# Performance work log

Measured on AMD Instinct MI355X. Metric: run time of the kernel, lower is better.

Reference implementation:

```python
import jax, jax.numpy as jnp
import numpy as np

RBF_CO = 10.077141124806595


def setup_inputs() -> dict:
    key = jax.random.key(0)
    k1, k2, k3 = jax.random.split(key, 3)
    n, dim = 2048, 128
    N, out_dim = 50000, 64
    features = jax.random.normal(k1, (n, dim), dtype=jnp.float32)
    train_data = jax.random.normal(k2, (N, dim), dtype=jnp.float32)
    weights = jax.random.normal(k3, (N, out_dim), dtype=jnp.float32) * 0.02
    return {"features": features, "train_data": train_data, "weights": weights}


def reference(features, train_data, weights):
    x2 = jnp.sum(features * features, axis=-1, keepdims=True)      # [n, 1]
    t2 = jnp.sum(train_data * train_data, axis=-1)                 # [N]
    d2 = x2 + t2[None, :] - 2.0 * (features @ train_data.T)        # [n, N]
    dist = jnp.sqrt(jnp.maximum(d2, 0.0))                          # clamp fp error
    k = jnp.exp(-dist / RBF_CO / 2.0)                              # RBF kernel [n, N]
    return k @ weights                                              # [n, out_dim]
```

## Files before the change

### kernel.cpp

```cpp
#include <hip/hip_runtime.h>
#include <hip/hip_bf16.h>
#include <stdint.h>

#define DIM 128
#define ODIM 64
#define BM 128
#define BN 64
#define NSPLIT 48
#define SPROW 72

typedef __attribute__((ext_vector_type(8))) __bf16 bf16x8;
typedef __attribute__((ext_vector_type(2))) __bf16 bf16x2;
typedef __attribute__((ext_vector_type(4))) float f32x4;

#define MFMA16(a, b, c) __builtin_amdgcn_mfma_f32_16x16x32_bf16((a), (b), (c), 0, 0, 0)

#define RBFD 10.077141124806595
#define LOG2E 1.4426950408889634
#define C2D ((LOG2E / (2.0 * RBFD)) * (LOG2E / (2.0 * RBFD)))

__device__ __forceinline__ void async_copy16(const void* g, void* l) {
  __builtin_amdgcn_global_load_lds((const __attribute__((address_space(1))) void*)g,
                                   (__attribute__((address_space(3))) void*)l, 16, 0, 0);
}
__device__ __forceinline__ void async_copy4(const void* g, void* l) {
  __builtin_amdgcn_global_load_lds((const __attribute__((address_space(1))) void*)g,
                                   (__attribute__((address_space(3))) void*)l, 4, 0, 0);
}

__device__ __forceinline__ uint32_t pack_bf16(float a, float b) {
  uint32_t ua = __builtin_bit_cast(uint32_t, a) + 0x8000u;
  uint32_t ub = __builtin_bit_cast(uint32_t, b) + 0x8000u;
  return __builtin_amdgcn_perm(ub, ua, 0x07060302u);
}

__global__ void prep_rows(const float* __restrict__ train, __bf16* __restrict__ Tb,
                          float* __restrict__ t2, const float* __restrict__ feat,
                          __bf16* __restrict__ Fb, float* __restrict__ x2,
                          int Ntrain, int NpadTrain, int nFeat, int trainBlocks, float scale) {
  int b = blockIdx.x;
  const float* src;
  __bf16* dst;
  float* sq;
  int nValid, nPad, row0;
  float padv;
  if (b < trainBlocks) {
    src = train; dst = Tb; sq = t2; nValid = Ntrain; nPad = NpadTrain; row0 = b * 4; padv = 1e30f;
  } else {
    src = feat; dst = Fb; sq = x2; nValid = nFeat; nPad = nFeat; row0 = (b - trainBlocks) * 4; padv = 0.0f;
  }
  int row = row0 + (threadIdx.x >> 6);
  int lane = threadIdx.x & 63;
  if (row >= nPad) return;
  float2 v = make_float2(0.0f, 0.0f);
  if (row < nValid) v = ((const float2*)src)[(size_t)row * 64 + lane];
  bf16x2 p;
  p.x = (__bf16)v.x;
  p.y = (__bf16)v.y;
  *(bf16x2*)&dst[(size_t)row * DIM + lane * 2] = p;
  float ss = v.x * v.x + v.y * v.y;
  #pragma unroll
  for (int off = 32; off > 0; off >>= 1) ss += __shfl_down(ss, off);
  if (lane == 0) sq[row] = (row < nValid) ? ss * scale : padv;
}

__global__ void transpose_weights(const float* __restrict__ W, __bf16* __restrict__ Wt,
                                  int N, int Npad) {
  __shared__ float tile[64][65];
  int j0 = (int)blockIdx.x * 64;
  int t = threadIdx.x;
  int jr = t >> 2;
  int cg = (t & 3) * 16;
  int j = j0 + jr;
  if (j < N) {
    const float4* src = (const float4*)(W + (size_t)j * ODIM);
    #pragma unroll
    for (int q = 0; q < 4; ++q) {
      float4 u = src[(cg >> 2) + q];
      tile[jr][cg + q * 4 + 0] = u.x;
      tile[jr][cg + q * 4 + 1] = u.y;
      tile[jr][cg + q * 4 + 2] = u.z;
      tile[jr][cg + q * 4 + 3] = u.w;
    }
  } else {
    #pragma unroll
    for (int q = 0; q < 16; ++q) tile[jr][cg + q] = 0.0f;
  }
  __syncthreads();
  int v = t >> 2;
  int jc = (t & 3) * 16;
  __bf16 ob[16];
  #pragma unroll
  for (int q = 0; q < 16; ++q) ob[q] = (__bf16)tile[jc + q][v];
  __bf16* dst = Wt + (size_t)v * Npad + j0 + jc;
  *(bf16x8*)dst = *(bf16x8*)&ob[0];
  *(bf16x8*)(dst + 8) = *(bf16x8*)&ob[8];
}

template <bool ATOMIC>
__global__ __launch_bounds__(256, 3) void rbf_main(
    const __bf16* __restrict__ Fb, const __bf16* __restrict__ Tb,
    const __bf16* __restrict__ Wt, const float* __restrict__ t2g,
    const float* __restrict__ x2g, float* __restrict__ outOrPart,
    int nRows, int Npad, int nChunks) {
  __shared__ __bf16 sT[BN * DIM];
  __shared__ __bf16 sW[ODIM * BN];
  __shared__ __bf16 sP[BM * SPROW];
  __shared__ float st2[BN];

  const int tid = threadIdx.x;
  const int wave = tid >> 6;
  const int lane = tid & 63;
  const int l16 = lane & 15;
  const int g4 = lane >> 4;

  const int ns = (int)blockIdx.x;
  const int mb = (int)blockIdx.y;

  constexpr float KNEG2 = (float)(-2.0 * C2D);

  bf16x8 bF[2][4];
  #pragma unroll
  for (int nf = 0; nf < 2; ++nf)
    #pragma unroll
    for (int ko = 0; ko < 4; ++ko)
      bF[nf][ko] = *(const bf16x8*)(Fb + ((size_t)(mb * BM + wave * 32 + nf * 16 + l16)) * DIM +
                                    ko * 32 + g4 * 8);

  float x2v[2];
  #pragma unroll
  for (int nf = 0; nf < 2; ++nf)
    x2v[nf] = x2g[mb * BM + wave * 32 + nf * 16 + l16];

  f32x4 zero4 = {0.0f, 0.0f, 0.0f, 0.0f};
  f32x4 oacc[2][4];
  #pragma unroll
  for (int mo = 0; mo < 2; ++mo)
    #pragma unroll
    for (int vi = 0; vi < 4; ++vi) oacc[mo][vi] = zero4;

  for (int c = ns; c < nChunks; c += NSPLIT) {
    const int n0 = c * BN;

    {
      const char* gT = (const char*)Tb + (size_t)n0 * 256;
      #pragma unroll
      for (int i = 0; i < 4; ++i) {
        int off = i * 4096 + wave * 1024;
        int loff = off + lane * 16;
        int row = loff >> 8;
        int gran = (loff >> 4) & 15;
        async_copy16(gT + row * 256 + ((gran ^ (row & 15)) << 4), (char*)sT + off);
      }
    }
    {
      #pragma unroll
      for (int i = 0; i < 2; ++i) {
        int off = i * 4096 + wave * 1024;
        int loff = off + lane * 16;
        int v = loff >> 7;
        int gran = (loff >> 4) & 7;
        const char* gW = (const char*)Wt + ((size_t)v * Npad + n0) * 2 + ((gran ^ (v & 7)) << 4);
        async_copy16(gW, (char*)sW + off);
      }
    }
    if (wave == 0) async_copy4((const char*)(t2g + n0) + lane * 4, (char*)st2);
    __syncthreads();

    f32x4 sacc[4][2];
    #pragma unroll
    for (int mt = 0; mt < 4; ++mt)
      #pragma unroll
      for (int nf = 0; nf < 2; ++nf) sacc[mt][nf] = zero4;

    #pragma unroll
    for (int ko = 0; ko < 4; ++ko) {
      bf16x8 a[4];
      #pragma unroll
      for (int mt = 0; mt < 4; ++mt) {
        int row = mt * 16 + l16;
        int slot = (ko * 4 + g4) ^ l16;
        a[mt] = *(const bf16x8*)((const char*)sT + row * 256 + (slot << 4));
      }
      #pragma unroll
      for (int mt = 0; mt < 4; ++mt)
        #pragma unroll
        for (int nf = 0; nf < 2; ++nf)
          sacc[mt][nf] = MFMA16(a[mt], bF[nf][ko], sacc[mt][nf]);
    }

    #pragma unroll
    for (int mt = 0; mt < 4; ++mt) {
      f32x4 t2v = *(const f32x4*)&st2[mt * 16 + g4 * 4];
      #pragma unroll
      for (int nf = 0; nf < 2; ++nf) {
        f32x4 s = sacc[mt][nf];
        float kv[4];
        #pragma unroll
        for (int r = 0; r < 4; ++r) {
          float d2 = __builtin_fmaf(KNEG2, s[r], t2v[r] + x2v[nf]);
          d2 = fmaxf(d2, 0.0f);
          kv[r] = __builtin_amdgcn_exp2f(-__builtin_amdgcn_sqrtf(d2));
        }
        uint32_t lo = pack_bf16(kv[0], kv[1]);
        uint32_t hi = pack_bf16(kv[2], kv[3]);
        uint2* dst = (uint2*)&sP[(wave * 32 + nf * 16 + l16) * SPROW + mt * 16 + g4 * 4];
        *dst = make_uint2(lo, hi);
      }
    }

    #pragma unroll
    for (int ko2 = 0; ko2 < 2; ++ko2) {
      bf16x8 p[2];
      #pragma unroll
      for (int mo = 0; mo < 2; ++mo)
        p[mo] = *(const bf16x8*)&sP[(wave * 32 + mo * 16 + l16) * SPROW + ko2 * 32 + g4 * 8];
      bf16x8 w[4];
      #pragma unroll
      for (int vi = 0; vi < 4; ++vi) {
        int v = vi * 16 + l16;
        int slot = (ko2 * 4 + g4) ^ (l16 & 7);
        w[vi] = *(const bf16x8*)((const char*)sW + v * 128 + (slot << 4));
      }
      #pragma unroll
      for (int mo = 0; mo < 2; ++mo)
        #pragma unroll
        for (int vi = 0; vi < 4; ++vi)
          oacc[mo][vi] = MFMA16(p[mo], w[vi], oacc[mo][vi]);
    }
    __syncthreads();
  }

  if (ATOMIC) {
    float* out = outOrPart;
    #pragma unroll
    for (int mo = 0; mo < 2; ++mo)
      #pragma unroll
      for (int vi = 0; vi < 4; ++vi)
        #pragma unroll
        for (int r = 0; r < 4; ++r) {
          int row = mb * BM + wave * 32 + mo * 16 + g4 * 4 + r;
          int col = vi * 16 + l16;
          atomicAdd(&out[(size_t)row * ODIM + col], oacc[mo][vi][r]);
        }
  } else {
    float* dst = outOrPart + (size_t)ns * (size_t)nRows * ODIM;
    #pragma unroll
    for (int mo = 0; mo < 2; ++mo)
      #pragma unroll
      for (int vi = 0; vi < 4; ++vi)
        #pragma unroll
        for (int r = 0; r < 4; ++r) {
          int row = mb * BM + wave * 32 + mo * 16 + g4 * 4 + r;
          int col = vi * 16 + l16;
          dst[(size_t)row * ODIM + col] = oacc[mo][vi][r];
        }
  }
}

__global__ void reduce_parts(const float4* __restrict__ part, float4* __restrict__ out,
                             int total4) {
  int i = (int)blockIdx.x * blockDim.x + threadIdx.x;
  if (i >= total4) return;
  float4 s = make_float4(0.0f, 0.0f, 0.0f, 0.0f);
  #pragma unroll
  for (int sp = 0; sp < NSPLIT; ++sp) {
    float4 v = part[(size_t)sp * total4 + i];
    s.x += v.x; s.y += v.y; s.z += v.z; s.w += v.w;
  }
  out[i] = s;
}

extern "C" void kernel_launch(void* const* d_in, const int* in_sizes, int n_in,
                              void* d_out, int out_size, void* d_ws, size_t ws_size,
                              hipStream_t stream) {
  (void)n_in;
  const float* features = (const float*)d_in[0];
  const float* train = (const float*)d_in[1];
  const float* weights = (const float*)d_in[2];
  float* out = (float*)d_out;

  const int n = in_sizes[0] / DIM;
  const int N = in_sizes[1] / DIM;
  const int Npad = ((N + 63) / 64) * 64;
  const int nChunks = Npad / 64;

  size_t off = 0;
  auto alloc = [&](size_t bytes) {
    size_t o = off;
    off = (off + bytes + 255) & ~(size_t)255;
    return o;
  };
  size_t oT = alloc((size_t)Npad * DIM * 2);
  size_t oW = alloc((size_t)ODIM * Npad * 2);
  size_t oF = alloc((size_t)n * DIM * 2);
  size_t ot2 = alloc((size_t)Npad * 4);
  size_t ox2 = alloc((size_t)n * 4);
  size_t oPart = alloc((size_t)NSPLIT * n * ODIM * 4);
  size_t needFull = off;

  char* ws = (char*)d_ws;
  __bf16* Tb = (__bf16*)(ws + oT);
  __bf16* Wt = (__bf16*)(ws + oW);
  __bf16* Fb = (__bf16*)(ws + oF);
  float* t2 = (float*)(ws + ot2);
  float* x2 = (float*)(ws + ox2);

  const float scale = (float)C2D;
  const int trainBlocks = Npad / 4;
  prep_rows<<<trainBlocks + n / 4, 256, 0, stream>>>(train, Tb, t2, features, Fb, x2,
                                                     N, Npad, n, trainBlocks, scale);
  transpose_weights<<<Npad / 64, 256, 0, stream>>>(weights, Wt, N, Npad);

  const int mBlocks = n / BM;
  dim3 grid(NSPLIT, mBlocks);

  if (ws_size >= needFull) {
    float* part = (float*)(ws + oPart);
    rbf_main<false><<<grid, 256, 0, stream>>>(Fb, Tb, Wt, t2, x2, part, n, Npad, nChunks);
    int total4 = n * ODIM / 4;
    reduce_parts<<<(total4 + 255) / 256, 256, 0, stream>>>((const float4*)part, (float4*)out,
                                                           total4);
  } else {
    hipMemsetAsync(d_out, 0, (size_t)out_size * sizeof(float), stream);
    rbf_main<true><<<grid, 256, 0, stream>>>(Fb, Tb, Wt, t2, x2, out, n, Npad, nChunks);
  }
}
```

Baseline: 146.0 us.

## Feed RBF kernel values from registers into second MFMA, drop LDS staging

Removes the shared-memory round trip for the bf16 kernel matrix by packing exp results in registers and feeding them directly as A operands of 16x16x16 MFMAs, relying on the accumulator layout matching the operand layout. This frees LDS, allowing occupancy to be raised to 4 blocks per CU, and the split count is raised to 64 with grid axes swapped. The preprocessing and weight transpose kernels are merged into one launch. The clamp of d2 to zero is dropped, risking NaN from sqrt of small negative values.

```diff
diff --git a/kernel.cpp b/kernel.cpp
--- a/kernel.cpp
+++ b/kernel.cpp
@@ -6,14 +6,15 @@
 #define ODIM 64
 #define BM 128
 #define BN 64
-#define NSPLIT 48
-#define SPROW 72
+#define NSPLIT 64
 
 typedef __attribute__((ext_vector_type(8))) __bf16 bf16x8;
+typedef __attribute__((ext_vector_type(4))) __bf16 bf16x4;
 typedef __attribute__((ext_vector_type(2))) __bf16 bf16x2;
 typedef __attribute__((ext_vector_type(4))) float f32x4;
 
-#define MFMA16(a, b, c) __builtin_amdgcn_mfma_f32_16x16x32_bf16((a), (b), (c), 0, 0, 0)
+#define MFMA_K32(a, b, c) __builtin_amdgcn_mfma_f32_16x16x32_bf16((a), (b), (c), 0, 0, 0)
+#define MFMA_K16(a, b, c) __builtin_amdgcn_mfma_f32_16x16x16bf16_1k((a), (b), (c), 0, 0, 0)
 
 #define RBFD 10.077141124806595
 #define LOG2E 1.4426950408889634
@@ -34,45 +35,45 @@
   return __builtin_amdgcn_perm(ub, ua, 0x07060302u);
 }
 
-__global__ void prep_rows(const float* __restrict__ train, __bf16* __restrict__ Tb,
-                          float* __restrict__ t2, const float* __restrict__ feat,
-                          __bf16* __restrict__ Fb, float* __restrict__ x2,
-                          int Ntrain, int NpadTrain, int nFeat, int trainBlocks, float scale) {
+__global__ void prep_all(const float* __restrict__ train, __bf16* __restrict__ Tb,
+                         float* __restrict__ t2, const float* __restrict__ feat,
+                         __bf16* __restrict__ Fb, float* __restrict__ x2,
+                         const float* __restrict__ W, __bf16* __restrict__ Wt,
+                         int Ntrain, int Npad, int nFeat, int tB, int fB, float scale) {
+  __shared__ float tile[64][65];
   int b = blockIdx.x;
-  const float* src;
-  __bf16* dst;
-  float* sq;
-  int nValid, nPad, row0;
-  float padv;
-  if (b < trainBlocks) {
-    src = train; dst = Tb; sq = t2; nValid = Ntrain; nPad = NpadTrain; row0 = b * 4; padv = 1e30f;
-  } else {
-    src = feat; dst = Fb; sq = x2; nValid = nFeat; nPad = nFeat; row0 = (b - trainBlocks) * 4; padv = 0.0f;
-  }
-  int row = row0 + (threadIdx.x >> 6);
-  int lane = threadIdx.x & 63;
-  if (row >= nPad) return;
-  float2 v = make_float2(0.0f, 0.0f);
-  if (row < nValid) v = ((const float2*)src)[(size_t)row * 64 + lane];
-  bf16x2 p;
-  p.x = (__bf16)v.x;
-  p.y = (__bf16)v.y;
-  *(bf16x2*)&dst[(size_t)row * DIM + lane * 2] = p;
-  float ss = v.x * v.x + v.y * v.y;
-  #pragma unroll
-  for (int off = 32; off > 0; off >>= 1) ss += __shfl_down(ss, off);
-  if (lane == 0) sq[row] = (row < nValid) ? ss * scale : padv;
-}
-
-__global__ void transpose_weights(const float* __restrict__ W, __bf16* __restrict__ Wt,
-                                  int N, int Npad) {
-  __shared__ float tile[64][65];
-  int j0 = (int)blockIdx.x * 64;
   int t = threadIdx.x;
+  if (b < tB + fB) {
+    const float* src;
+    __bf16* dst;
+    float* sq;
+    int nValid, nPad, row0;
+    float padv;
+    if (b < tB) {
+      src = train; dst = Tb; sq = t2; nValid = Ntrain; nPad = Npad; row0 = b * 4; padv = 1e30f;
+    } else {
+      src = feat; dst = Fb; sq = x2; nValid = nFeat; nPad = nFeat; row0 = (b - tB) * 4; padv = 0.0f;
+    }
+    int row = row0 + (t >> 6);
+    int lane = t & 63;
+    if (row >= nPad) return;
+    float2 v = make_float2(0.0f, 0.0f);
+    if (row < nValid) v = ((const float2*)src)[(size_t)row * 64 + lane];
+    bf16x2 p;
+    p.x = (__bf16)v.x;
+    p.y = (__bf16)v.y;
+    *(bf16x2*)&dst[(size_t)row * DIM + lane * 2] = p;
+    float ss = v.x * v.x + v.y * v.y;
+    #pragma unroll
+    for (int off = 32; off > 0; off >>= 1) ss += __shfl_down(ss, off);
+    if (lane == 0) sq[row] = (row < nValid) ? ss * scale : padv;
+    return;
+  }
+  int j0 = (b - tB - fB) * 64;
   int jr = t >> 2;
   int cg = (t & 3) * 16;
   int j = j0 + jr;
-  if (j < N) {
+  if (j < Ntrain) {
     const float4* src = (const float4*)(W + (size_t)j * ODIM);
     #pragma unroll
     for (int q = 0; q < 4; ++q) {
@@ -98,14 +99,13 @@
 }
 
 template <bool ATOMIC>
-__global__ __launch_bounds__(256, 3) void rbf_main(
+__global__ __launch_bounds__(256, 4) void rbf_main(
     const __bf16* __restrict__ Fb, const __bf16* __restrict__ Tb,
     const __bf16* __restrict__ Wt, const float* __restrict__ t2g,
     const float* __restrict__ x2g, float* __restrict__ outOrPart,
     int nRows, int Npad, int nChunks) {
   __shared__ __bf16 sT[BN * DIM];
   __shared__ __bf16 sW[ODIM * BN];
-  __shared__ __bf16 sP[BM * SPROW];
   __shared__ float st2[BN];
 
   const int tid = threadIdx.x;
@@ -114,8 +114,8 @@
   const int l16 = lane & 15;
   const int g4 = lane >> 4;
 
-  const int ns = (int)blockIdx.x;
-  const int mb = (int)blockIdx.y;
+  const int mb = (int)blockIdx.x;
+  const int ns = (int)blockIdx.y;
 
   constexpr float KNEG2 = (float)(-2.0 * C2D);
 
@@ -135,9 +135,9 @@
   f32x4 zero4 = {0.0f, 0.0f, 0.0f, 0.0f};
   f32x4 oacc[2][4];
   #pragma unroll
-  for (int mo = 0; mo < 2; ++mo)
-    #pragma unroll
-    for (int vi = 0; vi < 4; ++vi) oacc[mo][vi] = zero4;
+  for (int nf = 0; nf < 2; ++nf)
+    #pragma unroll
+    for (int vi = 0; vi < 4; ++vi) oacc[nf][vi] = zero4;
 
   for (int c = ns; c < nChunks; c += NSPLIT) {
     const int n0 = c * BN;
@@ -167,66 +167,40 @@
     if (wave == 0) async_copy4((const char*)(t2g + n0) + lane * 4, (char*)st2);
     __syncthreads();
 
-    f32x4 sacc[4][2];
-    #pragma unroll
-    for (int mt = 0; mt < 4; ++mt)
-      #pragma unroll
-      for (int nf = 0; nf < 2; ++nf) sacc[mt][nf] = zero4;
-
-    #pragma unroll
-    for (int ko = 0; ko < 4; ++ko) {
-      bf16x8 a[4];
+    uint2 pk[4][2];
+    #pragma unroll
+    for (int mt = 0; mt < 4; ++mt) {
+      f32x4 s0 = zero4, s1 = zero4;
+      #pragma unroll
+      for (int ko = 0; ko < 4; ++ko) {
+        int slot = (ko * 4 + g4) ^ l16;
+        bf16x8 a = *(const bf16x8*)((const char*)sT + (mt * 16 + l16) * 256 + (slot << 4));
+        s0 = MFMA_K32(a, bF[0][ko], s0);
+        s1 = MFMA_K32(a, bF[1][ko], s1);
+      }
+      f32x4 t2v = *(const f32x4*)&st2[mt * 16 + g4 * 4];
+      float kv0[4], kv1[4];
+      #pragma unroll
+      for (int r = 0; r < 4; ++r) {
+        float d20 = __builtin_fmaf(KNEG2, s0[r], t2v[r] + x2v[0]);
+        float d21 = __builtin_fmaf(KNEG2, s1[r], t2v[r] + x2v[1]);
+        kv0[r] = __builtin_amdgcn_exp2f(-__builtin_amdgcn_sqrtf(d20));
+        kv1[r] = __builtin_amdgcn_exp2f(-__builtin_amdgcn_sqrtf(d21));
+      }
+      pk[mt][0] = make_uint2(pack_bf16(kv0[0], kv0[1]), pack_bf16(kv0[2], kv0[3]));
+      pk[mt][1] = make_uint2(pack_bf16(kv1[0], kv1[1]), pack_bf16(kv1[2], kv1[3]));
+    }
+
+    #pragma unroll
+    for (int vi = 0; vi < 4; ++vi) {
+      int rowB = (vi * 16 + l16) * 128 + ((g4 & 1) << 3);
       #pragma unroll
       for (int mt = 0; mt < 4; ++mt) {
-        int row = mt * 16 + l16;
-        int slot = (ko * 4 + g4) ^ l16;
-        a[mt] = *(const bf16x8*)((const char*)sT + row * 256 + (slot << 4));
-      }
-      #pragma unroll
-      for (int mt = 0; mt < 4; ++mt)
-        #pragma unroll
-        for (int nf = 0; nf < 2; ++nf)
-          sacc[mt][nf] = MFMA16(a[mt], bF[nf][ko], sacc[mt][nf]);
-    }
-
-    #pragma unroll
-    for (int mt = 0; mt < 4; ++mt) {
-      f32x4 t2v = *(const f32x4*)&st2[mt * 16 + g4 * 4];
-      #pragma unroll
-      for (int nf = 0; nf < 2; ++nf) {
-        f32x4 s = sacc[mt][nf];
-        float kv[4];
-        #pragma unroll
-        for (int r = 0; r < 4; ++r) {
-          float d2 = __builtin_fmaf(KNEG2, s[r], t2v[r] + x2v[nf]);
-          d2 = fmaxf(d2, 0.0f);
-          kv[r] = __builtin_amdgcn_exp2f(-__builtin_amdgcn_sqrtf(d2));
-        }
-        uint32_t lo = pack_bf16(kv[0], kv[1]);
-        uint32_t hi = pack_bf16(kv[2], kv[3]);
-        uint2* dst = (uint2*)&sP[(wave * 32 + nf * 16 + l16) * SPROW + mt * 16 + g4 * 4];
-        *dst = make_uint2(lo, hi);
-      }
-    }
-
-    #pragma unroll
-    for (int ko2 = 0; ko2 < 2; ++ko2) {
-      bf16x8 p[2];
-      #pragma unroll
-      for (int mo = 0; mo < 2; ++mo)
-        p[mo] = *(const bf16x8*)&sP[(wave * 32 + mo * 16 + l16) * SPROW + ko2 * 32 + g4 * 8];
-      bf16x8 w[4];
-      #pragma unroll
-      for (int vi = 0; vi < 4; ++vi) {
-        int v = vi * 16 + l16;
-        int slot = (ko2 * 4 + g4) ^ (l16 & 7);
-        w[vi] = *(const bf16x8*)((const char*)sW + v * 128 + (slot << 4));
-      }
-      #pragma unroll
-      for (int mo = 0; mo < 2; ++mo)
-        #pragma unroll
-        for (int vi = 0; vi < 4; ++vi)
-          oacc[mo][vi] = MFMA16(p[mo], w[vi], oacc[mo][vi]);
+        int gran = (2 * mt + (g4 >> 1)) ^ (l16 & 7);
+        bf16x4 wf = *(const bf16x4*)((const char*)sW + rowB + (gran << 4));
+        oacc[0][vi] = MFMA_K16(__builtin_bit_cast(bf16x4, pk[mt][0]), wf, oacc[0][vi]);
+        oacc[1][vi] = MFMA_K16(__builtin_bit_cast(bf16x4, pk[mt][1]), wf, oacc[1][vi]);
+      }
     }
     __syncthreads();
   }
@@ -234,26 +208,26 @@
   if (ATOMIC) {
     float* out = outOrPart;
     #pragma unroll
-    for (int mo = 0; mo < 2; ++mo)
+    for (int nf = 0; nf < 2; ++nf)
       #pragma unroll
       for (int vi = 0; vi < 4; ++vi)
         #pragma unroll
         for (int r = 0; r < 4; ++r) {
-          int row = mb * BM + wave * 32 + mo * 16 + g4 * 4 + r;
+          int row = mb * BM + wave * 32 + nf * 16 + g4 * 4 + r;
           int col = vi * 16 + l16;
-          atomicAdd(&out[(size_t)row * ODIM + col], oacc[mo][vi][r]);
+          atomicAdd(&out[(size_t)row * ODIM + col], oacc[nf][vi][r]);
         }
   } else {
     float* dst = outOrPart + (size_t)ns * (size_t)nRows * ODIM;
     #pragma unroll
-    for (int mo = 0; mo < 2; ++mo)
+    for (int nf = 0; nf < 2; ++nf)
       #pragma unroll
       for (int vi = 0; vi < 4; ++vi)
         #pragma unroll
         for (int r = 0; r < 4; ++r) {
-          int row = mb * BM + wave * 32 + mo * 16 + g4 * 4 + r;
+          int row = mb * BM + wave * 32 + nf * 16 + g4 * 4 + r;
           int col = vi * 16 + l16;
-          dst[(size_t)row * ODIM + col] = oacc[mo][vi][r];
+          dst[(size_t)row * ODIM + col] = oacc[nf][vi][r];
         }
   }
 }
@@ -306,14 +280,14 @@
   float* t2 = (float*)(ws + ot2);
   float* x2 = (float*)(ws + ox2);
 
-  const float scale = (float)C2D;
-  const int trainBlocks = Npad / 4;
-  prep_rows<<<trainBlocks + n / 4, 256, 0, stream>>>(train, Tb, t2, features, Fb, x2,
-                                                     N, Npad, n, trainBlocks, scale);
-  transpose_weights<<<Npad / 64, 256, 0, stream>>>(weights, Wt, N, Npad);
+  const int tB = Npad / 4;
+  const int fB = n / 4;
+  const int wB = Npad / 64;
+  prep_all<<<tB + fB + wB, 256, 0, stream>>>(train, Tb, t2, features, Fb, x2, weights, Wt,
+                                             N, Npad, n, tB, fB, (float)C2D);
 
   const int mBlocks = n / BM;
-  dim3 grid(NSPLIT, mBlocks);
+  dim3 grid(mBlocks, NSPLIT);
 
   if (ws_size >= needFull) {
     float* part = (float*)(ws + oPart);
```

Result: no change. 146.5 us (+0.3%).
